# Kernel optimization log

Measured on AMD Instinct MI355X. Metric: run time of the kernel, lower is better.

Reference implementation:

```python
import jax, jax.numpy as jnp
import numpy as np

B, T, D_IN = 128, 256, 128
HID = 256
NUM_CLASSES = 250
LN_EPS = 1e-5


def _gru_dir(x, Wih, Whh, bih, bhh, reverse):
    """Single-direction GRU over [B,T,Din] -> [B,T,H] (PyTorch gate math)."""
    # Precompute input projections for all timesteps in one big GEMM.
    gx = jnp.einsum('btd,gd->btg', x, Wih) + bih  # [B,T,3H]
    if reverse:
        gx = gx[:, ::-1]
    H = Whh.shape[1]
    Whr, Whz, Whn = jnp.split(Whh, 3, axis=0)
    br, bz, bn = jnp.split(bhh, 3)
    h0 = jnp.zeros((x.shape[0], H), x.dtype)

    def step(h, gxt):
        xr, xz, xn = jnp.split(gxt, 3, axis=-1)
        r = jax.nn.sigmoid(xr + h @ Whr.T + br)
        z = jax.nn.sigmoid(xz + h @ Whz.T + bz)
        n = jnp.tanh(xn + r * (h @ Whn.T + bn))
        h_new = (1.0 - z) * n + z * h
        return h_new, h_new

    _, ys = jax.lax.scan(step, h0, jnp.swapaxes(gx, 0, 1))  # [T,B,H]
    ys = jnp.swapaxes(ys, 0, 1)  # [B,T,H]
    if reverse:
        ys = ys[:, ::-1]
    return ys


def _bidir_layer(x, wf, whf, bf, bhf, wr, whr, br_, bhr):
    fwd = _gru_dir(x, wf, whf, bf, bhf, reverse=False)
    bwd = _gru_dir(x, wr, whr, br_, bhr, reverse=True)
    return jnp.concatenate([fwd, bwd], axis=-1)  # [B,T,2H]


def setup_inputs() -> dict:
    key = jax.random.key(0)
    ks = jax.random.split(key, 24)
    k = 1.0 / np.sqrt(HID)

    def u(kk, shape, bound):
        return jax.random.uniform(kk, shape, jnp.float32, -bound, bound)

    inp = {"x": jax.random.normal(ks[0], (B, T, D_IN), jnp.float32)}
    # layer 0 (input dim D_IN), layer 1 (input dim 2*HID); fwd + reverse dirs
    inp["w_ih_l0"]  = u(ks[1], (3 * HID, D_IN), k)
    inp["w_hh_l0"]  = u(ks[2], (3 * HID, HID), k)
    inp["b_ih_l0"]  = u(ks[3], (3 * HID,), k)
    inp["b_hh_l0"]  = u(ks[4], (3 * HID,), k)
    inp["w_ih_l0r"] = u(ks[5], (3 * HID, D_IN), k)
    inp["w_hh_l0r"] = u(ks[6], (3 * HID, HID), k)
    inp["b_ih_l0r"] = u(ks[7], (3 * HID,), k)
    inp["b_hh_l0r"] = u(ks[8], (3 * HID,), k)
    inp["w_ih_l1"]  = u(ks[9], (3 * HID, 2 * HID), k)
    inp["w_hh_l1"]  = u(ks[10], (3 * HID, HID), k)
    inp["b_ih_l1"]  = u(ks[11], (3 * HID,), k)
    inp["b_hh_l1"]  = u(ks[12], (3 * HID,), k)
    inp["w_ih_l1r"] = u(ks[13], (3 * HID, 2 * HID), k)
    inp["w_hh_l1r"] = u(ks[14], (3 * HID, HID), k)
    inp["b_ih_l1r"] = u(ks[15], (3 * HID,), k)
    inp["b_hh_l1r"] = u(ks[16], (3 * HID,), k)
    inp["ln_g"] = jnp.ones((2 * HID,), jnp.float32)
    inp["ln_b"] = jnp.zeros((2 * HID,), jnp.float32)
    kh = 1.0 / np.sqrt(2 * HID)
    inp["head_w"] = u(ks[17], (NUM_CLASSES, 2 * HID), kh)
    inp["head_b"] = u(ks[18], (NUM_CLASSES,), kh)
    return inp


def reference(x, w_ih_l0, w_hh_l0, b_ih_l0, b_hh_l0,
              w_ih_l0r, w_hh_l0r, b_ih_l0r, b_hh_l0r,
              w_ih_l1, w_hh_l1, b_ih_l1, b_hh_l1,
              w_ih_l1r, w_hh_l1r, b_ih_l1r, b_hh_l1r,
              ln_g, ln_b, head_w, head_b):
    # 2-layer bidirectional GRU (eval mode: inter-layer dropout is identity)
    h1 = _bidir_layer(x, w_ih_l0, w_hh_l0, b_ih_l0, b_hh_l0,
                      w_ih_l0r, w_hh_l0r, b_ih_l0r, b_hh_l0r)
    h2 = _bidir_layer(h1, w_ih_l1, w_hh_l1, b_ih_l1, b_hh_l1,
                      w_ih_l1r, w_hh_l1r, b_ih_l1r, b_hh_l1r)
    last = h2[:, -1, :]  # [B, 2H]
    mu = jnp.mean(last, axis=-1, keepdims=True)
    var = jnp.mean((last - mu) ** 2, axis=-1, keepdims=True)
    normed = (last - mu) * jax.lax.rsqrt(var + LN_EPS) * ln_g + ln_b
    logits = normed @ head_w.T + head_b  # [B, num_classes]
    return logits
```

## Files before the change

kernel.cpp:

```cpp
#include <hip/hip_runtime.h>
#include <math.h>

#define B_SZ 128
#define T_SZ 256
#define DIN  128
#define HID  256
#define H2   512
#define NCLS 250

typedef float    f32x4 __attribute__((ext_vector_type(4)));
typedef unsigned u32x4 __attribute__((ext_vector_type(4)));

__device__ __forceinline__ void tg_load1(const unsigned* p, u32x4& a) {
    asm volatile("global_load_dwordx4 %0, %1, off sc0 sc1\n\t"
                 "s_waitcnt vmcnt(0)"
                 : "=&v"(a) : "v"(p) : "memory");
}
__device__ __forceinline__ void tg_load2_split(const unsigned* p, u32x4& a, u32x4& b) {
    asm volatile("global_load_dwordx4 %0, %2, off sc0 sc1\n\t"
                 "global_load_dwordx4 %1, %2, off offset:512 sc0 sc1\n\t"
                 "s_waitcnt vmcnt(0)"
                 : "=&v"(a), "=&v"(b) : "v"(p) : "memory");
}
__device__ __forceinline__ void tg_store4(unsigned* p, u32x4 v) {
    asm volatile("global_store_dwordx4 %0, %1, off sc0 sc1" :: "v"(p), "v"(v) : "memory");
}

#define ACC4(A, Wp, v) \
    A = fmaf((v).x, (Wp)[0], A); A = fmaf((v).y, (Wp)[1], A); \
    A = fmaf((v).z, (Wp)[2], A); A = fmaf((v).w, (Wp)[3], A)

__device__ __forceinline__ void group_decode(int wg, int& g, int& member) {
    member = (wg >> 3) & 15;
    g = (wg & 7) * 4 + (wg >> 7);
}

__global__ __launch_bounds__(256, 2) void l0_scan(
    const float* __restrict__ x,
    const float* __restrict__ wihf, const float* __restrict__ bihf,
    const float* __restrict__ whhf, const float* __restrict__ bhhf,
    const float* __restrict__ wihb, const float* __restrict__ bihb,
    const float* __restrict__ whhb, const float* __restrict__ bhhb,
    unsigned* __restrict__ thb,
    float* __restrict__ h1)
{
    __shared__ float hlds[8][256];
    __shared__ float xlds[2][8][128];
    __shared__ float hst[8][20];
    const int tid = threadIdx.x;
    int g, member;
    group_decode(blockIdx.x, g, member);
    const int dir = g >> 4;
    const int b0  = (g & 15) * 8;
    const int hct = member;
    const int hc = tid >> 4, ks = tid & 15, ks4 = ks * 4;
    const int hcg = hct * 16 + hc;

    const float* wih = dir ? wihb : wihf;
    const float* bih = dir ? bihb : bihf;
    const float* whh = dir ? whhb : whhf;
    const float* bhh = dir ? bhhb : bhhf;

    float Wr[3][16], Wx[3][8];
#pragma unroll
    for (int gg = 0; gg < 3; ++gg) {
#pragma unroll
        for (int j = 0; j < 4; ++j) {
            float4 wv = *(const float4*)(whh + (size_t)(gg * HID + hcg) * HID + j * 64 + ks4);
            Wr[gg][4 * j] = wv.x; Wr[gg][4 * j + 1] = wv.y; Wr[gg][4 * j + 2] = wv.z; Wr[gg][4 * j + 3] = wv.w;
        }
#pragma unroll
        for (int j = 0; j < 2; ++j) {
            float4 wv = *(const float4*)(wih + (size_t)(gg * HID + hcg) * DIN + j * 64 + ks4);
            Wx[gg][4 * j] = wv.x; Wx[gg][4 * j + 1] = wv.y; Wx[gg][4 * j + 2] = wv.z; Wx[gg][4 * j + 3] = wv.w;
        }
    }
    const float sbr = bih[hcg] + bhh[hcg];
    const float sbz = bih[HID + hcg] + bhh[HID + hcg];
    const float bxn = bih[2 * HID + hcg];
    const float bhn = bhh[2 * HID + hcg];

    unsigned* hb = thb + (size_t)dir * 2 * B_SZ * HID;
    const int r8 = tid >> 5, c32 = (tid & 31) * 4;
    const int prow = tid >> 5, pc4 = (tid & 31) * 4;

    float4 xp;
    {
        const int tg0 = dir ? (T_SZ - 1) : 0;
        xp = *(const float4*)(x + ((size_t)(b0 + r8) * T_SZ + tg0) * DIN + c32);
        *(float4*)&xlds[0][r8][c32] = xp;
    }
    __syncthreads();
    {
        const int tg1 = dir ? (T_SZ - 2) : 1;
        xp = *(const float4*)(x + ((size_t)(b0 + r8) * T_SZ + tg1) * DIN + c32);
    }
    float xsr[8], xsz[8], xsn[8];
#pragma unroll
    for (int b = 0; b < 8; ++b) { xsr[b] = 0.f; xsz[b] = 0.f; xsn[b] = 0.f; }
#pragma unroll
    for (int b = 0; b < 8; ++b)
#pragma unroll
        for (int j = 0; j < 2; ++j) {
            float4 xv = *(const float4*)&xlds[0][b][j * 64 + ks4];
            ACC4(xsr[b], &Wx[0][4 * j], xv);
            ACC4(xsz[b], &Wx[1][4 * j], xv);
            ACC4(xsn[b], &Wx[2][4 * j], xv);
        }
#pragma unroll
    for (int m = 1; m <= 8; m <<= 1)
#pragma unroll
        for (int b = 0; b < 8; ++b) {
            xsr[b] += __shfl_xor(xsr[b], m, 64);
            xsz[b] += __shfl_xor(xsz[b], m, 64);
            xsn[b] += __shfl_xor(xsn[b], m, 64);
        }

    for (int t = 0; t < T_SZ; ++t) {
        const int tg = dir ? (T_SZ - 1 - t) : t;
        const unsigned* hp_t = hb + (size_t)(t & 1) * B_SZ * HID;
        unsigned* hn_t       = hb + (size_t)((t + 1) & 1) * B_SZ * HID;
        const unsigned tgv = (unsigned)(t & 3);
        const unsigned wtv = (unsigned)((t + 1) & 3);

        {
            const unsigned* pp = hp_t + (size_t)(b0 + prow) * HID + pc4;
            u32x4 va, vb;
            for (;;) {
                tg_load2_split(pp, va, vb);
                unsigned m = (va.x^tgv)|(va.y^tgv)|(va.z^tgv)|(va.w^tgv)
                           | (vb.x^tgv)|(vb.y^tgv)|(vb.z^tgv)|(vb.w^tgv);
                if ((m & 3u) == 0u) break;
            }
            *(u32x4*)&hlds[prow][pc4]       = va;
            *(u32x4*)&hlds[prow][pc4 + 128] = vb;
        }
        *(float4*)&xlds[(t + 1) & 1][r8][c32] = xp;
        __syncthreads();

        {
            const int tn  = (t + 2 < T_SZ) ? (t + 2) : (T_SZ - 1);
            const int tgn = dir ? (T_SZ - 1 - tn) : tn;
            xp = *(const float4*)(x + ((size_t)(b0 + r8) * T_SZ + tgn) * DIN + c32);
        }

        float aR[8], aZ[8], aH[8];
#pragma unroll
        for (int b = 0; b < 8; ++b) { aR[b] = 0.f; aZ[b] = 0.f; aH[b] = 0.f; }
#pragma unroll
        for (int b = 0; b < 8; ++b)
#pragma unroll
            for (int j = 0; j < 4; ++j) {
                float4 hv4 = *(const float4*)&hlds[b][j * 64 + ks4];
                ACC4(aR[b], &Wr[0][4 * j], hv4);
                ACC4(aZ[b], &Wr[1][4 * j], hv4);
                ACC4(aH[b], &Wr[2][4 * j], hv4);
            }
#pragma unroll
        for (int m = 1; m <= 8; m <<= 1)
#pragma unroll
            for (int b = 0; b < 8; ++b) {
                aR[b] += __shfl_xor(aR[b], m, 64);
                aZ[b] += __shfl_xor(aZ[b], m, 64);
                aH[b] += __shfl_xor(aH[b], m, 64);
            }

        if (ks < 8) {
            float sr = 0.f, sz = 0.f, sh = 0.f, xr = 0.f, xz = 0.f, xn = 0.f;
#pragma unroll
            for (int b = 0; b < 8; ++b)
                if (b == ks) { sr = aR[b]; sz = aZ[b]; sh = aH[b];
                               xr = xsr[b]; xz = xsz[b]; xn = xsn[b]; }
            const float hp = hlds[ks][hcg];
            const float r = 1.f / (1.f + expf(-(sr + xr + sbr)));
            const float z = 1.f / (1.f + expf(-(sz + xz + sbz)));
            const float n = tanhf(xn + bxn + r * (sh + bhn));
            hst[ks][hc] = (1.f - z) * n + z * hp;
        }
        __syncthreads();
        if (tid < 32) {
            const int sr_ = tid >> 2, sc_ = (tid & 3) * 4;
            float4 hv4 = *(const float4*)&hst[sr_][sc_];
            u32x4 w;
            w.x = (__float_as_uint(hv4.x) & ~3u) | wtv;
            w.y = (__float_as_uint(hv4.y) & ~3u) | wtv;
            w.z = (__float_as_uint(hv4.z) & ~3u) | wtv;
            w.w = (__float_as_uint(hv4.w) & ~3u) | wtv;
            tg_store4(hn_t + (size_t)(b0 + sr_) * HID + hct * 16 + sc_, w);
            *(float4*)(h1 + ((size_t)(b0 + sr_) * T_SZ + tg) * H2 + dir * HID + hct * 16 + sc_) = hv4;
        }

#pragma unroll
        for (int b = 0; b < 8; ++b) { xsr[b] = 0.f; xsz[b] = 0.f; xsn[b] = 0.f; }
#pragma unroll
        for (int b = 0; b < 8; ++b)
#pragma unroll
            for (int j = 0; j < 2; ++j) {
                float4 xv = *(const float4*)&xlds[(t + 1) & 1][b][j * 64 + ks4];
                ACC4(xsr[b], &Wx[0][4 * j], xv);
                ACC4(xsz[b], &Wx[1][4 * j], xv);
                ACC4(xsn[b], &Wx[2][4 * j], xv);
            }
#pragma unroll
        for (int m = 1; m <= 8; m <<= 1)
#pragma unroll
            for (int b = 0; b < 8; ++b) {
                xsr[b] += __shfl_xor(xsr[b], m, 64);
                xsz[b] += __shfl_xor(xsz[b], m, 64);
                xsn[b] += __shfl_xor(xsn[b], m, 64);
            }
    }
}

__global__ __launch_bounds__(256, 2) void l1_scan(
    const float* __restrict__ h1,
    const float* __restrict__ wih, const float* __restrict__ bih,
    const float* __restrict__ whh, const float* __restrict__ bhh,
    unsigned* __restrict__ thb)
{
    __shared__ float hlds[4][256];
    __shared__ float xlds[2][4][512];
    __shared__ float hst[4][20];
    const int tid = threadIdx.x;
    int g, member;
    group_decode(blockIdx.x, g, member);
    const int b0  = g * 4;
    const int hct = member;
    const int hc = tid >> 4, ks = tid & 15, ks4 = ks * 4;
    const int hcg = hct * 16 + hc;

    float Wr[3][16], Wx[3][32];
#pragma unroll
    for (int gg = 0; gg < 3; ++gg) {
#pragma unroll
        for (int j = 0; j < 4; ++j) {
            float4 wv = *(const float4*)(whh + (size_t)(gg * HID + hcg) * HID + j * 64 + ks4);
            Wr[gg][4 * j] = wv.x; Wr[gg][4 * j + 1] = wv.y; Wr[gg][4 * j + 2] = wv.z; Wr[gg][4 * j + 3] = wv.w;
        }
#pragma unroll
        for (int j = 0; j < 8; ++j) {
            float4 wv = *(const float4*)(wih + (size_t)(gg * HID + hcg) * H2 + j * 64 + ks4);
            Wx[gg][4 * j] = wv.x; Wx[gg][4 * j + 1] = wv.y; Wx[gg][4 * j + 2] = wv.z; Wx[gg][4 * j + 3] = wv.w;
        }
    }
    const float sbr = bih[hcg] + bhh[hcg];
    const float sbz = bih[HID + hcg] + bhh[HID + hcg];
    const float bxn = bih[2 * HID + hcg];
    const float bhn = bhh[2 * HID + hcg];

    const int r4 = tid >> 6, s64 = (tid & 63) * 4;
    const int prw = tid >> 6, pc0 = (tid & 63) * 4;

    float4 xp[2];
    {
        const float* xsrc = h1 + ((size_t)(b0 + r4) * T_SZ + 0) * H2;
        xp[0] = *(const float4*)(xsrc + s64);
        xp[1] = *(const float4*)(xsrc + 256 + s64);
        *(float4*)&xlds[0][r4][s64]       = xp[0];
        *(float4*)&xlds[0][r4][256 + s64] = xp[1];
    }
    __syncthreads();
    {
        const float* xsrc = h1 + ((size_t)(b0 + r4) * T_SZ + 1) * H2;
        xp[0] = *(const float4*)(xsrc + s64);
        xp[1] = *(const float4*)(xsrc + 256 + s64);
    }
    float xsr[4], xsz[4], xsn[4];
#pragma unroll
    for (int b = 0; b < 4; ++b) { xsr[b] = 0.f; xsz[b] = 0.f; xsn[b] = 0.f; }
#pragma unroll
    for (int b = 0; b < 4; ++b)
#pragma unroll
        for (int j = 0; j < 8; ++j) {
            float4 xv = *(const float4*)&xlds[0][b][j * 64 + ks4];
            ACC4(xsr[b], &Wx[0][4 * j], xv);
            ACC4(xsz[b], &Wx[1][4 * j], xv);
            ACC4(xsn[b], &Wx[2][4 * j], xv);
        }
#pragma unroll
    for (int m = 1; m <= 8; m <<= 1)
#pragma unroll
        for (int b = 0; b < 4; ++b) {
            xsr[b] += __shfl_xor(xsr[b], m, 64);
            xsz[b] += __shfl_xor(xsz[b], m, 64);
            xsn[b] += __shfl_xor(xsn[b], m, 64);
        }

    for (int t = 0; t < T_SZ; ++t) {
        const unsigned* hp_t = thb + (size_t)(t & 1) * B_SZ * HID;
        unsigned* hn_t       = thb + (size_t)((t + 1) & 1) * B_SZ * HID;
        const unsigned tgv = (unsigned)(t & 3);
        const unsigned wtv = (unsigned)((t + 1) & 3);

        {
            const unsigned* pp = hp_t + (size_t)(b0 + prw) * HID + pc0;
            u32x4 va;
            for (;;) {
                tg_load1(pp, va);
                unsigned m = (va.x^tgv)|(va.y^tgv)|(va.z^tgv)|(va.w^tgv);
                if ((m & 3u) == 0u) break;
            }
            *(u32x4*)&hlds[prw][pc0] = va;
        }
        *(float4*)&xlds[(t + 1) & 1][r4][s64]       = xp[0];
        *(float4*)&xlds[(t + 1) & 1][r4][256 + s64] = xp[1];
        __syncthreads();

        {
            const int tn = (t + 2 < T_SZ) ? (t + 2) : (T_SZ - 1);
            const float* xsrc = h1 + ((size_t)(b0 + r4) * T_SZ + tn) * H2;
            xp[0] = *(const float4*)(xsrc + s64);
            xp[1] = *(const float4*)(xsrc + 256 + s64);
        }

        float aR[4], aZ[4], aH[4];
#pragma unroll
        for (int b = 0; b < 4; ++b) { aR[b] = 0.f; aZ[b] = 0.f; aH[b] = 0.f; }
#pragma unroll
        for (int b = 0; b < 4; ++b)
#pragma unroll
            for (int j = 0; j < 4; ++j) {
                float4 hv4 = *(const float4*)&hlds[b][j * 64 + ks4];
                ACC4(aR[b], &Wr[0][4 * j], hv4);
                ACC4(aZ[b], &Wr[1][4 * j], hv4);
                ACC4(aH[b], &Wr[2][4 * j], hv4);
            }
#pragma unroll
        for (int m = 1; m <= 8; m <<= 1)
#pragma unroll
            for (int b = 0; b < 4; ++b) {
                aR[b] += __shfl_xor(aR[b], m, 64);
                aZ[b] += __shfl_xor(aZ[b], m, 64);
                aH[b] += __shfl_xor(aH[b], m, 64);
            }

        if (ks < 4) {
            float sr = 0.f, sz = 0.f, sh = 0.f, xr = 0.f, xz = 0.f, xn = 0.f;
#pragma unroll
            for (int b = 0; b < 4; ++b)
                if (b == ks) { sr = aR[b]; sz = aZ[b]; sh = aH[b];
                               xr = xsr[b]; xz = xsz[b]; xn = xsn[b]; }
            const float hp = hlds[ks][hcg];
            const float r = 1.f / (1.f + expf(-(sr + xr + sbr)));
            const float z = 1.f / (1.f + expf(-(sz + xz + sbz)));
            const float n = tanhf(xn + bxn + r * (sh + bhn));
            hst[ks][hc] = (1.f - z) * n + z * hp;
        }
        __syncthreads();
        if (tid < 16) {
            const int sr_ = tid >> 2, sc_ = (tid & 3) * 4;
            float4 hv4 = *(const float4*)&hst[sr_][sc_];
            u32x4 w;
            w.x = (__float_as_uint(hv4.x) & ~3u) | wtv;
            w.y = (__float_as_uint(hv4.y) & ~3u) | wtv;
            w.z = (__float_as_uint(hv4.z) & ~3u) | wtv;
            w.w = (__float_as_uint(hv4.w) & ~3u) | wtv;
            tg_store4(hn_t + (size_t)(b0 + sr_) * HID + hct * 16 + sc_, w);
        }

#pragma unroll
        for (int b = 0; b < 4; ++b) { xsr[b] = 0.f; xsz[b] = 0.f; xsn[b] = 0.f; }
#pragma unroll
        for (int b = 0; b < 4; ++b)
#pragma unroll
            for (int j = 0; j < 8; ++j) {
                float4 xv = *(const float4*)&xlds[(t + 1) & 1][b][j * 64 + ks4];
                ACC4(xsr[b], &Wx[0][4 * j], xv);
                ACC4(xsz[b], &Wx[1][4 * j], xv);
                ACC4(xsn[b], &Wx[2][4 * j], xv);
            }
#pragma unroll
        for (int m = 1; m <= 8; m <<= 1)
#pragma unroll
            for (int b = 0; b < 4; ++b) {
                xsr[b] += __shfl_xor(xsr[b], m, 64);
                xsz[b] += __shfl_xor(xsz[b], m, 64);
                xsn[b] += __shfl_xor(xsn[b], m, 64);
            }
    }
}

__global__ __launch_bounds__(256) void l1r_laststep(
    const float* __restrict__ h1, const float* __restrict__ wih,
    const float* __restrict__ bih, const float* __restrict__ bhh,
    float* __restrict__ h2b)
{
    const int tid = threadIdx.x;
    const int b  = (blockIdx.x >> 4) * 16 + (tid >> 4);
    const int hc = (blockIdx.x & 15) * 16 + (tid & 15);
    const float* hrow = h1 + ((size_t)b * T_SZ + (T_SZ - 1)) * H2;
    float ar = 0.f, az = 0.f, an = 0.f;
#pragma unroll 8
    for (int k = 0; k < H2; k += 4) {
        float4 hv = *(const float4*)(hrow + k);
        float4 wr = *(const float4*)(wih + (size_t)hc * H2 + k);
        float4 wz = *(const float4*)(wih + (size_t)(HID + hc) * H2 + k);
        float4 wn = *(const float4*)(wih + (size_t)(2 * HID + hc) * H2 + k);
        ar = fmaf(hv.x, wr.x, fmaf(hv.y, wr.y, fmaf(hv.z, wr.z, fmaf(hv.w, wr.w, ar))));
        az = fmaf(hv.x, wz.x, fmaf(hv.y, wz.y, fmaf(hv.z, wz.z, fmaf(hv.w, wz.w, az))));
        an = fmaf(hv.x, wn.x, fmaf(hv.y, wn.y, fmaf(hv.z, wn.z, fmaf(hv.w, wn.w, an))));
    }
    float r = 1.f / (1.f + expf(-(ar + bih[hc] + bhh[hc])));
    float z = 1.f / (1.f + expf(-(az + bih[HID + hc] + bhh[HID + hc])));
    float n = tanhf(an + bih[2 * HID + hc] + r * bhh[2 * HID + hc]);
    h2b[(size_t)b * HID + hc] = (1.f - z) * n;
}

__global__ __launch_bounds__(256) void ln_head(
    const float* __restrict__ h2f, const float* __restrict__ h2b,
    const float* __restrict__ g, const float* __restrict__ be,
    const float* __restrict__ hw, const float* __restrict__ hb,
    float* __restrict__ out)
{
    __shared__ float v[H2];
    __shared__ float rbuf[8];
    const int b = blockIdx.x, tid = threadIdx.x;
    float xa = h2f[(size_t)b * HID + tid];
    float xb = h2b[(size_t)b * HID + tid];
    float s = xa + xb;
#pragma unroll
    for (int m = 32; m >= 1; m >>= 1) s += __shfl_xor(s, m, 64);
    if ((tid & 63) == 0) rbuf[tid >> 6] = s;
    __syncthreads();
    float mu = (rbuf[0] + rbuf[1] + rbuf[2] + rbuf[3]) * (1.0f / H2);
    float da = xa - mu, db = xb - mu;
    float q = da * da + db * db;
#pragma unroll
    for (int m = 32; m >= 1; m >>= 1) q += __shfl_xor(q, m, 64);
    __syncthreads();
    if ((tid & 63) == 0) rbuf[tid >> 6] = q;
    __syncthreads();
    float var = (rbuf[0] + rbuf[1] + rbuf[2] + rbuf[3]) * (1.0f / H2);
    float rs = rsqrtf(var + 1e-5f);
    v[tid]       = da * rs * g[tid] + be[tid];
    v[HID + tid] = db * rs * g[HID + tid] + be[HID + tid];
    __syncthreads();
    if (tid < NCLS) {
        float a = hb[tid];
        const float* wr = hw + (size_t)tid * H2;
#pragma unroll 4
        for (int k = 0; k < H2; k += 4) {
            float4 wv = *(const float4*)(wr + k);
            a = fmaf(v[k], wv.x, fmaf(v[k + 1], wv.y, fmaf(v[k + 2], wv.z, fmaf(v[k + 3], wv.w, a))));
        }
        out[(size_t)b * NCLS + tid] = a;
    }
}

extern "C" void kernel_launch(void* const* d_in, const int* in_sizes, int n_in,
                              void* d_out, int out_size, void* d_ws, size_t ws_size,
                              hipStream_t stream)
{
    const float* x     = (const float*)d_in[0];
    const float* wih0f = (const float*)d_in[1];
    const float* whh0f = (const float*)d_in[2];
    const float* bih0f = (const float*)d_in[3];
    const float* bhh0f = (const float*)d_in[4];
    const float* wih0b = (const float*)d_in[5];
    const float* whh0b = (const float*)d_in[6];
    const float* bih0b = (const float*)d_in[7];
    const float* bhh0b = (const float*)d_in[8];
    const float* wih1f = (const float*)d_in[9];
    const float* whh1f = (const float*)d_in[10];
    const float* bih1f = (const float*)d_in[11];
    const float* bhh1f = (const float*)d_in[12];
    const float* wih1b = (const float*)d_in[13];
    const float* whh1b = (const float*)d_in[14];
    const float* bih1b = (const float*)d_in[15];
    const float* bhh1b = (const float*)d_in[16];
    const float* lng   = (const float*)d_in[17];
    const float* lnb   = (const float*)d_in[18];
    const float* hw    = (const float*)d_in[19];
    const float* hbb   = (const float*)d_in[20];

    char* wsb = (char*)d_ws;
    size_t off = 0;
    auto alloc = [&](size_t bytes) -> void* {
        void* p = (void*)(wsb + off);
        off += (bytes + 255) & ~(size_t)255;
        return p;
    };
    unsigned* thbA = (unsigned*)alloc((size_t)2 * 2 * B_SZ * HID * 4);
    unsigned* thbB = (unsigned*)alloc((size_t)2 * B_SZ * HID * 4);
    size_t zspan = off;
    float* h2b = (float*)alloc((size_t)B_SZ * HID * 4);
    float* h1  = (float*)alloc((size_t)B_SZ * T_SZ * H2 * 4);

    (void)hipMemsetAsync(d_ws, 0, zspan, stream);

    l0_scan<<<dim3(512), dim3(256), 0, stream>>>(
        x, wih0f, bih0f, whh0f, bhh0f, wih0b, bih0b, whh0b, bhh0b, thbA, h1);

    l1r_laststep<<<dim3(128), dim3(256), 0, stream>>>(h1, wih1b, bih1b, bhh1b, h2b);

    l1_scan<<<dim3(512), dim3(256), 0, stream>>>(
        h1, wih1f, bih1f, whh1f, bhh1f, thbB);

    ln_head<<<dim3(B_SZ), dim3(256), 0, stream>>>(
        (const float*)thbB, h2b, lng, lnb, hw, hbb, (float*)d_out);
}
```

Baseline: 2.775 ms.

## Split layer-0 scan into 4-row batch groups across 1024 workgroups

The layer-0 bidirectional scan now gives each workgroup 4 batch rows instead of 8 and launches 1024 workgroups with launch bounds raised to 4 per CU. Per-step work per workgroup roughly halves (fewer FMAs, one 16-byte polled load per thread instead of two), which should shorten the serial critical path of each timestep. In exchange the grid doubles, so more workgroups spin on the global tagged handoff buffer, and every workgroup must stay co-resident for the spin-wait scheme to avoid deadlock.

```diff
diff --git a/kernel.cpp b/kernel.cpp
--- a/kernel.cpp
+++ b/kernel.cpp
@@ -16,12 +16,6 @@
                  "s_waitcnt vmcnt(0)"
                  : "=&v"(a) : "v"(p) : "memory");
 }
-__device__ __forceinline__ void tg_load2_split(const unsigned* p, u32x4& a, u32x4& b) {
-    asm volatile("global_load_dwordx4 %0, %2, off sc0 sc1\n\t"
-                 "global_load_dwordx4 %1, %2, off offset:512 sc0 sc1\n\t"
-                 "s_waitcnt vmcnt(0)"
-                 : "=&v"(a), "=&v"(b) : "v"(p) : "memory");
-}
 __device__ __forceinline__ void tg_store4(unsigned* p, u32x4 v) {
     asm volatile("global_store_dwordx4 %0, %1, off sc0 sc1" :: "v"(p), "v"(v) : "memory");
 }
@@ -30,12 +24,16 @@
     A = fmaf((v).x, (Wp)[0], A); A = fmaf((v).y, (Wp)[1], A); \
     A = fmaf((v).z, (Wp)[2], A); A = fmaf((v).w, (Wp)[3], A)
 
-__device__ __forceinline__ void group_decode(int wg, int& g, int& member) {
+__device__ __forceinline__ void group_decode_1024(int wg, int& g, int& member) {
+    member = (wg >> 3) & 15;
+    g = (wg & 7) * 8 + (wg >> 7);
+}
+__device__ __forceinline__ void group_decode_512(int wg, int& g, int& member) {
     member = (wg >> 3) & 15;
     g = (wg & 7) * 4 + (wg >> 7);
 }
 
-__global__ __launch_bounds__(256, 2) void l0_scan(
+__global__ __launch_bounds__(256, 4) void l0_scan(
     const float* __restrict__ x,
     const float* __restrict__ wihf, const float* __restrict__ bihf,
     const float* __restrict__ whhf, const float* __restrict__ bhhf,
@@ -44,14 +42,14 @@
     unsigned* __restrict__ thb,
     float* __restrict__ h1)
 {
-    __shared__ float hlds[8][256];
-    __shared__ float xlds[2][8][128];
-    __shared__ float hst[8][20];
+    __shared__ float hlds[4][256];
+    __shared__ float xlds[2][4][128];
+    __shared__ float hst[4][20];
     const int tid = threadIdx.x;
     int g, member;
-    group_decode(blockIdx.x, g, member);
-    const int dir = g >> 4;
-    const int b0  = (g & 15) * 8;
+    group_decode_1024(blockIdx.x, g, member);
+    const int dir = g >> 5;
+    const int b0  = (g & 31) * 4;
     const int hct = member;
     const int hc = tid >> 4, ks = tid & 15, ks4 = ks * 4;
     const int hcg = hct * 16 + hc;
@@ -81,25 +79,25 @@
     const float bhn = bhh[2 * HID + hcg];
 
     unsigned* hb = thb + (size_t)dir * 2 * B_SZ * HID;
-    const int r8 = tid >> 5, c32 = (tid & 31) * 4;
-    const int prow = tid >> 5, pc4 = (tid & 31) * 4;
+    const int xr_ = tid >> 5, xc = (tid & 31) * 4;
+    const int prw = tid >> 6, pc0 = (tid & 63) * 4;
 
     float4 xp;
-    {
+    if (tid < 128) {
         const int tg0 = dir ? (T_SZ - 1) : 0;
-        xp = *(const float4*)(x + ((size_t)(b0 + r8) * T_SZ + tg0) * DIN + c32);
-        *(float4*)&xlds[0][r8][c32] = xp;
-    }
-    __syncthreads();
-    {
+        xp = *(const float4*)(x + ((size_t)(b0 + xr_) * T_SZ + tg0) * DIN + xc);
+        *(float4*)&xlds[0][xr_][xc] = xp;
+    }
+    __syncthreads();
+    if (tid < 128) {
         const int tg1 = dir ? (T_SZ - 2) : 1;
-        xp = *(const float4*)(x + ((size_t)(b0 + r8) * T_SZ + tg1) * DIN + c32);
-    }
-    float xsr[8], xsz[8], xsn[8];
-#pragma unroll
-    for (int b = 0; b < 8; ++b) { xsr[b] = 0.f; xsz[b] = 0.f; xsn[b] = 0.f; }
-#pragma unroll
-    for (int b = 0; b < 8; ++b)
+        xp = *(const float4*)(x + ((size_t)(b0 + xr_) * T_SZ + tg1) * DIN + xc);
+    }
+    float xsr[4], xsz[4], xsn[4];
+#pragma unroll
+    for (int b = 0; b < 4; ++b) { xsr[b] = 0.f; xsz[b] = 0.f; xsn[b] = 0.f; }
+#pragma unroll
+    for (int b = 0; b < 4; ++b)
 #pragma unroll
         for (int j = 0; j < 2; ++j) {
             float4 xv = *(const float4*)&xlds[0][b][j * 64 + ks4];
@@ -110,7 +108,7 @@
 #pragma unroll
     for (int m = 1; m <= 8; m <<= 1)
 #pragma unroll
-        for (int b = 0; b < 8; ++b) {
+        for (int b = 0; b < 4; ++b) {
             xsr[b] += __shfl_xor(xsr[b], m, 64);
             xsz[b] += __shfl_xor(xsz[b], m, 64);
             xsn[b] += __shfl_xor(xsn[b], m, 64);
@@ -124,31 +122,30 @@
         const unsigned wtv = (unsigned)((t + 1) & 3);
 
         {
-            const unsigned* pp = hp_t + (size_t)(b0 + prow) * HID + pc4;
-            u32x4 va, vb;
+            const unsigned* pp = hp_t + (size_t)(b0 + prw) * HID + pc0;
+            u32x4 va;
             for (;;) {
-                tg_load2_split(pp, va, vb);
-                unsigned m = (va.x^tgv)|(va.y^tgv)|(va.z^tgv)|(va.w^tgv)
-                           | (vb.x^tgv)|(vb.y^tgv)|(vb.z^tgv)|(vb.w^tgv);
+                tg_load1(pp, va);
+                unsigned m = (va.x^tgv)|(va.y^tgv)|(va.z^tgv)|(va.w^tgv);
                 if ((m & 3u) == 0u) break;
             }
-            *(u32x4*)&hlds[prow][pc4]       = va;
-            *(u32x4*)&hlds[prow][pc4 + 128] = vb;
-        }
-        *(float4*)&xlds[(t + 1) & 1][r8][c32] = xp;
+            *(u32x4*)&hlds[prw][pc0] = va;
+        }
+        if (tid < 128)
+            *(float4*)&xlds[(t + 1) & 1][xr_][xc] = xp;
         __syncthreads();
 
-        {
+        if (tid < 128) {
             const int tn  = (t + 2 < T_SZ) ? (t + 2) : (T_SZ - 1);
             const int tgn = dir ? (T_SZ - 1 - tn) : tn;
-            xp = *(const float4*)(x + ((size_t)(b0 + r8) * T_SZ + tgn) * DIN + c32);
-        }
-
-        float aR[8], aZ[8], aH[8];
-#pragma unroll
-        for (int b = 0; b < 8; ++b) { aR[b] = 0.f; aZ[b] = 0.f; aH[b] = 0.f; }
-#pragma unroll
-        for (int b = 0; b < 8; ++b)
+            xp = *(const float4*)(x + ((size_t)(b0 + xr_) * T_SZ + tgn) * DIN + xc);
+        }
+
+        float aR[4], aZ[4], aH[4];
+#pragma unroll
+        for (int b = 0; b < 4; ++b) { aR[b] = 0.f; aZ[b] = 0.f; aH[b] = 0.f; }
+#pragma unroll
+        for (int b = 0; b < 4; ++b)
 #pragma unroll
             for (int j = 0; j < 4; ++j) {
                 float4 hv4 = *(const float4*)&hlds[b][j * 64 + ks4];
@@ -159,16 +156,16 @@
 #pragma unroll
         for (int m = 1; m <= 8; m <<= 1)
 #pragma unroll
-            for (int b = 0; b < 8; ++b) {
+            for (int b = 0; b < 4; ++b) {
                 aR[b] += __shfl_xor(aR[b], m, 64);
                 aZ[b] += __shfl_xor(aZ[b], m, 64);
                 aH[b] += __shfl_xor(aH[b], m, 64);
             }
 
-        if (ks < 8) {
+        if (ks < 4) {
             float sr = 0.f, sz = 0.f, sh = 0.f, xr = 0.f, xz = 0.f, xn = 0.f;
 #pragma unroll
-            for (int b = 0; b < 8; ++b)
+            for (int b = 0; b < 4; ++b)
                 if (b == ks) { sr = aR[b]; sz = aZ[b]; sh = aH[b];
                                xr = xsr[b]; xz = xsz[b]; xn = xsn[b]; }
             const float hp = hlds[ks][hcg];
@@ -178,7 +175,7 @@
             hst[ks][hc] = (1.f - z) * n + z * hp;
         }
         __syncthreads();
-        if (tid < 32) {
+        if (tid < 16) {
             const int sr_ = tid >> 2, sc_ = (tid & 3) * 4;
             float4 hv4 = *(const float4*)&hst[sr_][sc_];
             u32x4 w;
@@ -191,9 +188,9 @@
         }
 
 #pragma unroll
-        for (int b = 0; b < 8; ++b) { xsr[b] = 0.f; xsz[b] = 0.f; xsn[b] = 0.f; }
-#pragma unroll
-        for (int b = 0; b < 8; ++b)
+        for (int b = 0; b < 4; ++b) { xsr[b] = 0.f; xsz[b] = 0.f; xsn[b] = 0.f; }
+#pragma unroll
+        for (int b = 0; b < 4; ++b)
 #pragma unroll
             for (int j = 0; j < 2; ++j) {
                 float4 xv = *(const float4*)&xlds[(t + 1) & 1][b][j * 64 + ks4];
@@ -204,7 +201,7 @@
 #pragma unroll
         for (int m = 1; m <= 8; m <<= 1)
 #pragma unroll
-            for (int b = 0; b < 8; ++b) {
+            for (int b = 0; b < 4; ++b) {
                 xsr[b] += __shfl_xor(xsr[b], m, 64);
                 xsz[b] += __shfl_xor(xsz[b], m, 64);
                 xsn[b] += __shfl_xor(xsn[b], m, 64);
@@ -223,7 +220,7 @@
     __shared__ float hst[4][20];
     const int tid = threadIdx.x;
     int g, member;
-    group_decode(blockIdx.x, g, member);
+    group_decode_512(blockIdx.x, g, member);
     const int b0  = g * 4;
     const int hct = member;
     const int hc = tid >> 4, ks = tid & 15, ks4 = ks * 4;
@@ -488,7 +485,7 @@
 
     (void)hipMemsetAsync(d_ws, 0, zspan, stream);
 
-    l0_scan<<<dim3(512), dim3(256), 0, stream>>>(
+    l0_scan<<<dim3(1024), dim3(256), 0, stream>>>(
         x, wih0f, bih0f, whh0f, bhh0f, wih0b, bih0b, whh0b, bhh0b, thbA, h1);
 
     l1r_laststep<<<dim3(128), dim3(256), 0, stream>>>(h1, wih1b, bih1b, bhh1b, h2b);
```

Result: slower. 3.572 ms (+28.7%).
